# Performance work log

Hardware: AMD Instinct MI355X
Metric: run time of the kernel (lower is better)

Reference implementation:

```python
import jax, jax.numpy as jnp
import numpy as np

POOL = 7
NUM_ROIS = 256
SCALE = 1.0 / 16.0  # feature-map stride
H, W, C = 128, 128, 1024
STRIDE = 16


def setup_inputs() -> dict:
    key = jax.random.key(0)
    k_img, k_wh, k_xy = jax.random.split(key, 3)
    img = jax.random.normal(k_img, (1, H, W, C), dtype=jnp.float32)
    # ROIs in image-pixel units (x, y, w, h); w,h >= 16 so crop >= 1 feature cell
    max_px = H * STRIDE  # 2048
    wh = jax.random.uniform(k_wh, (1, NUM_ROIS, 2), minval=16.0, maxval=max_px * 0.5)
    xy = jax.random.uniform(k_xy, (1, NUM_ROIS, 2), minval=0.0, maxval=1.0) * (max_px - wh)
    rois = jnp.concatenate([xy, wh], axis=-1).astype(jnp.float32)
    return {"img": img, "rois": rois}


def _pool_one_roi(img0, roi):
    # img0: (H, W, C); roi: (4,) = (x, y, w, h) in pixels.
    # Original: int cast of scaled coords, crop img[y:y+h, x:x+w],
    # then TF1 bilinear resize (align_corners=False, src = i * in/out).
    c = (roi * SCALE).astype(jnp.int32)  # truncation == floor for positive coords
    x0, y0, w, h = c[0], c[1], c[2], c[3]
    i = jnp.arange(POOL, dtype=jnp.float32)
    # source coords within the cropped section
    sy = i * (h.astype(jnp.float32) / POOL)
    sx = i * (w.astype(jnp.float32) / POOL)
    fy = jnp.floor(sy)
    fx = jnp.floor(sx)
    ty = sy - fy  # (P,) lerp weights
    tx = sx - fx
    y_lo = fy.astype(jnp.int32)
    x_lo = fx.astype(jnp.int32)
    y_hi = jnp.minimum(y_lo + 1, jnp.maximum(h - 1, 0))  # clamp at section edge
    x_hi = jnp.minimum(x_lo + 1, jnp.maximum(w - 1, 0))
    gy0 = jnp.clip(y0 + y_lo, 0, H - 1)
    gy1 = jnp.clip(y0 + y_hi, 0, H - 1)
    gx0 = jnp.clip(x0 + x_lo, 0, W - 1)
    gx1 = jnp.clip(x0 + x_hi, 0, W - 1)
    v00 = img0[gy0[:, None], gx0[None, :]]  # (P, P, C)
    v01 = img0[gy0[:, None], gx1[None, :]]
    v10 = img0[gy1[:, None], gx0[None, :]]
    v11 = img0[gy1[:, None], gx1[None, :]]
    top = v00 + tx[None, :, None] * (v01 - v00)
    bot = v10 + tx[None, :, None] * (v11 - v10)
    return top + ty[:, None, None] * (bot - top)  # (P, P, C)


def reference(img, rois):
    img0 = img[0]  # (H, W, C)
    pooled = jax.vmap(lambda r: _pool_one_roi(img0, r))(rois[0])  # (NR, P, P, C)
    return pooled[None]  # (1, num_rois, pool, pool, C)
```

## Files before the change

kernel.cpp:

```cpp
#include <hip/hip_runtime.h>


#define IMG_H 128
#define IMG_W 128
#define IMG_C 1024
#define POOLK 7
#define NROIS 256

typedef float vfloat4 __attribute__((ext_vector_type(4)));

__global__ __launch_bounds__(256, 4) void roi_pool_kernel(
    const float* __restrict__ img,
    const float* __restrict__ rois,
    float* __restrict__ out) {
  const int iy = blockIdx.x;
  const int r  = blockIdx.y;

  const vfloat4 roi = *(const vfloat4*)(rois + (size_t)r * 4);

  const int x0 = (int)(roi.x * 0.0625f);
  const int y0 = (int)(roi.y * 0.0625f);
  const int w  = (int)(roi.z * 0.0625f);
  const int h  = (int)(roi.w * 0.0625f);

  const float sy = (float)iy * ((float)h * (1.0f / 7.0f));
  const float fy = floorf(sy);
  const float ty = sy - fy;
  const int y_lo = (int)fy;
  const int y_hi = min(y_lo + 1, max(h - 1, 0));
  const int gy0 = min(max(y0 + y_lo, 0), IMG_H - 1);
  const int gy1 = min(max(y0 + y_hi, 0), IMG_H - 1);

  const int c = threadIdx.x * 4;
  const float* row0 = img + (size_t)gy0 * (IMG_W * IMG_C) + c;
  const float* row1 = img + (size_t)gy1 * (IMG_W * IMG_C) + c;
  float* orow = out + (((size_t)r * POOLK + iy) * POOLK) * IMG_C + c;

  const float step_x = (float)w * (1.0f / 7.0f);
  const int xmax = max(w - 1, 0);

  float tx_c = 0.0f;
  const int gx0_0 = min(max(x0, 0), IMG_W - 1);
  const int gx1_0 = min(max(x0 + min(1, xmax), 0), IMG_W - 1);
  vfloat4 v00 = *(const vfloat4*)(row0 + (size_t)gx0_0 * IMG_C);
  vfloat4 v01 = *(const vfloat4*)(row0 + (size_t)gx1_0 * IMG_C);
  vfloat4 v10 = *(const vfloat4*)(row1 + (size_t)gx0_0 * IMG_C);
  vfloat4 v11 = *(const vfloat4*)(row1 + (size_t)gx1_0 * IMG_C);

#pragma unroll
  for (int ix = 0; ix < POOLK; ++ix) {
    vfloat4 n00{}, n01{}, n10{}, n11{};
    float tx_n = 0.0f;
    if (ix + 1 < POOLK) {
      const float sx = (float)(ix + 1) * step_x;
      const float fx = floorf(sx);
      tx_n = sx - fx;
      const int x_lo = (int)fx;
      const int x_hi = min(x_lo + 1, xmax);
      const int gx0 = min(max(x0 + x_lo, 0), IMG_W - 1);
      const int gx1 = min(max(x0 + x_hi, 0), IMG_W - 1);
      n00 = *(const vfloat4*)(row0 + (size_t)gx0 * IMG_C);
      n01 = *(const vfloat4*)(row0 + (size_t)gx1 * IMG_C);
      n10 = *(const vfloat4*)(row1 + (size_t)gx0 * IMG_C);
      n11 = *(const vfloat4*)(row1 + (size_t)gx1 * IMG_C);
    }

    const vfloat4 top = v00 + tx_c * (v01 - v00);
    const vfloat4 bot = v10 + tx_c * (v11 - v10);
    const vfloat4 o   = top + ty * (bot - top);
    __builtin_nontemporal_store(o, (vfloat4*)(orow + (size_t)ix * IMG_C));

    v00 = n00; v01 = n01; v10 = n10; v11 = n11; tx_c = tx_n;
  }
}

extern "C" void kernel_launch(void* const* d_in, const int* in_sizes, int n_in,
                              void* d_out, int out_size, void* d_ws, size_t ws_size,
                              hipStream_t stream) {
  const float* img  = (const float*)d_in[0];
  const float* rois = (const float*)d_in[1];
  float* out = (float*)d_out;

  dim3 grid(POOLK, NROIS);
  dim3 block(256);
  roi_pool_kernel<<<grid, block, 0, stream>>>(img, rois, out);
}
```

Baseline: 120.2 us.

## Remap blocks per XCD, force scalar address math, raise occupancy bound

After: 119.1 us. Within noise of the previous version (-0.9%).

```diff
diff --git a/kernel.cpp b/kernel.cpp
--- a/kernel.cpp
+++ b/kernel.cpp
@@ -6,22 +6,27 @@
 #define IMG_C 1024
 #define POOLK 7
 #define NROIS 256
+#define NBLK (POOLK * NROIS)
+#define NXCD 8
+#define CHUNK (NBLK / NXCD)
 
 typedef float vfloat4 __attribute__((ext_vector_type(4)));
 
-__global__ __launch_bounds__(256, 4) void roi_pool_kernel(
+__global__ __launch_bounds__(256, 8) void roi_pool_kernel(
     const float* __restrict__ img,
     const float* __restrict__ rois,
     float* __restrict__ out) {
-  const int iy = blockIdx.x;
-  const int r  = blockIdx.y;
+  const int orig = (int)blockIdx.x;
+  const int newb = (orig & (NXCD - 1)) * CHUNK + (orig >> 3);
+  const int r  = newb / POOLK;
+  const int iy = newb - r * POOLK;
 
   const vfloat4 roi = *(const vfloat4*)(rois + (size_t)r * 4);
 
-  const int x0 = (int)(roi.x * 0.0625f);
-  const int y0 = (int)(roi.y * 0.0625f);
-  const int w  = (int)(roi.z * 0.0625f);
-  const int h  = (int)(roi.w * 0.0625f);
+  const int x0 = __builtin_amdgcn_readfirstlane((int)(roi.x * 0.0625f));
+  const int y0 = __builtin_amdgcn_readfirstlane((int)(roi.y * 0.0625f));
+  const int w  = __builtin_amdgcn_readfirstlane((int)(roi.z * 0.0625f));
+  const int h  = __builtin_amdgcn_readfirstlane((int)(roi.w * 0.0625f));
 
   const float sy = (float)iy * ((float)h * (1.0f / 7.0f));
   const float fy = floorf(sy);
@@ -31,21 +36,29 @@
   const int gy0 = min(max(y0 + y_lo, 0), IMG_H - 1);
   const int gy1 = min(max(y0 + y_hi, 0), IMG_H - 1);
 
-  const int c = threadIdx.x * 4;
-  const float* row0 = img + (size_t)gy0 * (IMG_W * IMG_C) + c;
-  const float* row1 = img + (size_t)gy1 * (IMG_W * IMG_C) + c;
+  const int row0_e = __builtin_amdgcn_readfirstlane(gy0 * (IMG_W * IMG_C));
+  const int row1_e = __builtin_amdgcn_readfirstlane(gy1 * (IMG_W * IMG_C));
+
+  const int c = (int)threadIdx.x * 4;
   float* orow = out + (((size_t)r * POOLK + iy) * POOLK) * IMG_C + c;
 
   const float step_x = (float)w * (1.0f / 7.0f);
   const int xmax = max(w - 1, 0);
 
   float tx_c = 0.0f;
+  {
+    const int gx0_0 = min(max(x0, 0), IMG_W - 1);
+    const int gx1_0 = min(max(x0 + min(1, xmax), 0), IMG_W - 1);
+    #define OFF(row_e, gx) ((size_t)__builtin_amdgcn_readfirstlane((row_e) + (gx) * IMG_C) + c)
+    ;
+    #undef OFF
+  }
   const int gx0_0 = min(max(x0, 0), IMG_W - 1);
   const int gx1_0 = min(max(x0 + min(1, xmax), 0), IMG_W - 1);
-  vfloat4 v00 = *(const vfloat4*)(row0 + (size_t)gx0_0 * IMG_C);
-  vfloat4 v01 = *(const vfloat4*)(row0 + (size_t)gx1_0 * IMG_C);
-  vfloat4 v10 = *(const vfloat4*)(row1 + (size_t)gx0_0 * IMG_C);
-  vfloat4 v11 = *(const vfloat4*)(row1 + (size_t)gx1_0 * IMG_C);
+  vfloat4 v00 = *(const vfloat4*)(img + (size_t)__builtin_amdgcn_readfirstlane(row0_e + gx0_0 * IMG_C) + c);
+  vfloat4 v01 = *(const vfloat4*)(img + (size_t)__builtin_amdgcn_readfirstlane(row0_e + gx1_0 * IMG_C) + c);
+  vfloat4 v10 = *(const vfloat4*)(img + (size_t)__builtin_amdgcn_readfirstlane(row1_e + gx0_0 * IMG_C) + c);
+  vfloat4 v11 = *(const vfloat4*)(img + (size_t)__builtin_amdgcn_readfirstlane(row1_e + gx1_0 * IMG_C) + c);
 
 #pragma unroll
   for (int ix = 0; ix < POOLK; ++ix) {
@@ -59,10 +72,10 @@
       const int x_hi = min(x_lo + 1, xmax);
       const int gx0 = min(max(x0 + x_lo, 0), IMG_W - 1);
       const int gx1 = min(max(x0 + x_hi, 0), IMG_W - 1);
-      n00 = *(const vfloat4*)(row0 + (size_t)gx0 * IMG_C);
-      n01 = *(const vfloat4*)(row0 + (size_t)gx1 * IMG_C);
-      n10 = *(const vfloat4*)(row1 + (size_t)gx0 * IMG_C);
-      n11 = *(const vfloat4*)(row1 + (size_t)gx1 * IMG_C);
+      n00 = *(const vfloat4*)(img + (size_t)__builtin_amdgcn_readfirstlane(row0_e + gx0 * IMG_C) + c);
+      n01 = *(const vfloat4*)(img + (size_t)__builtin_amdgcn_readfirstlane(row0_e + gx1 * IMG_C) + c);
+      n10 = *(const vfloat4*)(img + (size_t)__builtin_amdgcn_readfirstlane(row1_e + gx0 * IMG_C) + c);
+      n11 = *(const vfloat4*)(img + (size_t)__builtin_amdgcn_readfirstlane(row1_e + gx1 * IMG_C) + c);
     }
 
     const vfloat4 top = v00 + tx_c * (v01 - v00);
@@ -81,7 +94,7 @@
   const float* rois = (const float*)d_in[1];
   float* out = (float*)d_out;
 
-  dim3 grid(POOLK, NROIS);
+  dim3 grid(NBLK);
   dim3 block(256);
   roi_pool_kernel<<<grid, block, 0, stream>>>(img, rois, out);
 }
```
